# Optimization experiments

Measured on AMD Instinct MI355X. Metric: run time of the kernel, lower is better.

## Reference

```python
import jax, jax.numpy as jnp
import numpy as np

B, S, D, H = 1, 4096, 1024, 16
HD = D // H  # head_size = 64

def setup_inputs() -> dict:
    key = jax.random.key(0)
    ks = jax.random.split(key, 9)
    scale = 1.0 / np.sqrt(D)
    return {
        "x": jax.random.normal(ks[0], (B, S, D), jnp.float32),
        "Wq": jax.random.normal(ks[1], (D, D), jnp.float32) * scale,
        "bq": jax.random.normal(ks[2], (D,), jnp.float32) * 0.01,
        "Wk": jax.random.normal(ks[3], (D, D), jnp.float32) * scale,
        "bk": jax.random.normal(ks[4], (D,), jnp.float32) * 0.01,
        "Wv": jax.random.normal(ks[5], (D, D), jnp.float32) * scale,
        "bv": jax.random.normal(ks[6], (D,), jnp.float32) * 0.01,
        "Wo": jax.random.normal(ks[7], (D, D), jnp.float32) * scale,
        "bo": jax.random.normal(ks[8], (D,), jnp.float32) * 0.01,
    }

def _split_heads(t):
    # (B, S, D) -> (B, H, S, HD)
    return t.reshape(B, S, H, HD).transpose(0, 2, 1, 3)

def reference(x, Wq, bq, Wk, bk, Wv, bv, Wo, bo):
    q = _split_heads(x @ Wq + bq)
    k = _split_heads(x @ Wk + bk)
    v = _split_heads(x @ Wv + bv)
    # scores: (B, H, S, S), materialized as in the original naive attention
    scores = jnp.einsum('bhqd,bhkd->bhqk', q, k) / jnp.sqrt(jnp.asarray(HD, q.dtype))
    causal = jnp.tril(jnp.ones((S, S), dtype=bool))  # tril mask, broadcast over (B, H)
    scores = jnp.where(causal[None, None], scores, jnp.asarray(-1e9, scores.dtype))
    attn = jax.nn.softmax(scores, axis=-1)
    out = jnp.einsum('bhqk,bhkd->bhqd', attn, v)  # (B, H, S, HD)
    out = out.transpose(0, 2, 1, 3).reshape(B, S, D)  # combine heads
    return out @ Wo + bo
```

## Files before the change

### kernel.cpp

```cpp
#include <hip/hip_runtime.h>

#define SEQ 4096
#define DM  1024
#define NH  16
#define HDIM 64

typedef unsigned short u16;
typedef unsigned int   u32;
typedef __bf16 bf16x8 __attribute__((ext_vector_type(8)));
typedef float f32x4 __attribute__((ext_vector_type(4)));

__device__ __forceinline__ float bf2f(u16 u) {
    unsigned v = ((unsigned)u) << 16;
    float f;
    __builtin_memcpy(&f, &v, 4);
    return f;
}
__device__ __forceinline__ u16 f2bf(float f) {
    unsigned u;
    __builtin_memcpy(&u, &f, 4);
    return (u16)((u + 0x7fffu + ((u >> 16) & 1u)) >> 16);
}
__device__ __forceinline__ u32 bfpack(float a, float b) {
    u32 ua, ub;
    __builtin_memcpy(&ua, &a, 4);
    __builtin_memcpy(&ub, &b, 4);
    return ((ua + 0x8000u) >> 16) | ((ub + 0x8000u) & 0xffff0000u);
}

typedef const __attribute__((address_space(1))) unsigned int gas_uint;
typedef __attribute__((address_space(3))) unsigned int las_uint;
__device__ __forceinline__ void gld16(const u16* g, u16* l) {
    __builtin_amdgcn_global_load_lds((gas_uint*)g, (las_uint*)l, 16, 0, 0);
}

__device__ __forceinline__ f32x4 mfma16(bf16x8 a, bf16x8 b, f32x4 c) {
    return __builtin_amdgcn_mfma_f32_16x16x32_bf16(a, b, c, 0, 0, 0);
}

#define QSCALE 0.18033688011f

__global__ __launch_bounds__(256) void detect_k(const u16* __restrict__ w,
                                                int* __restrict__ flags) {
    __shared__ float red[256];
    const int t = threadIdx.x;
    float mx = 0.f;
    for (int i = t; i < 4096; i += 256) {
        float v = fabsf(bf2f(w[i]));
        if (v < 3e38f) mx = fmaxf(mx, v);
    }
    red[t] = mx;
    __syncthreads();
    for (int s = 128; s > 0; s >>= 1) {
        if (t < s) red[t] = fmaxf(red[t], red[t + s]);
        __syncthreads();
    }
    if (t == 0) {
        flags[0] = (red[0] > 1e4f) ? 1 : 0;
        flags[1] = 0;
    }
}

__global__ __launch_bounds__(256) void prep_w(const void* w0, const void* w1,
                                              const void* w2, const void* w3,
                                              const void* b0, const void* b1,
                                              const void* b2, const void* b3,
                                              u16* __restrict__ wt,
                                              u16* __restrict__ b_dst,
                                              const int* __restrict__ flags) {
    __shared__ u16 tile[32][33];
    const int f = flags[0];
    const int z = blockIdx.z;
    const void* win[4] = {w0, w1, w2, w3};
    const void* bin[4] = {b0, b1, b2, b3};
    const void* in = win[z];
    u16* out = wt + (size_t)z * DM * DM;
    const float scale = (z == 0) ? QSCALE : 1.0f;

    const int bx = blockIdx.x * 32;
    const int by = blockIdx.y * 32;
    const int tx = threadIdx.x & 31;
    const int ty = threadIdx.x >> 5;
#pragma unroll
    for (int i = ty; i < 32; i += 8) {
        size_t idx = (size_t)(by + i) * DM + bx + tx;
        float v = f ? ((const float*)in)[idx] : bf2f(((const u16*)in)[idx]);
        tile[i][tx] = f2bf(v * scale);
    }
    __syncthreads();
#pragma unroll
    for (int i = ty; i < 32; i += 8) out[(size_t)(bx + i) * DM + by + tx] = tile[tx][i];

    if (blockIdx.x == 0 && blockIdx.y == 0) {
        const void* bi = bin[z];
        for (int i = threadIdx.x; i < DM; i += 256) {
            float v = f ? ((const float*)bi)[i] : bf2f(((const u16*)bi)[i]);
            b_dst[z * DM + i] = f2bf(v * scale);
        }
    }
}

__global__ __launch_bounds__(256) void cvt_x8(const void* __restrict__ src,
                                              u16* __restrict__ dst,
                                              const int* __restrict__ flags) {
    const size_t i = ((size_t)blockIdx.x * 256 + threadIdx.x) * 8;
    if (flags[0]) {
        const float4* s4 = (const float4*)((const float*)src + i);
        float4 a = s4[0], b = s4[1];
        uint4 o;
        o.x = bfpack(a.x, a.y);
        o.y = bfpack(a.z, a.w);
        o.z = bfpack(b.x, b.y);
        o.w = bfpack(b.z, b.w);
        *(uint4*)(dst + i) = o;
    } else {
        *(uint4*)(dst + i) = *(const uint4*)((const u16*)src + i);
    }
}

__global__ __launch_bounds__(256, 2) void gemm128(const u16* __restrict__ A,
                                                  const u16* __restrict__ Bt,
                                                  const u16* __restrict__ bias,
                                                  void* __restrict__ C0,
                                                  void* __restrict__ C1,
                                                  void* __restrict__ C2,
                                                  int M, int N, int K,
                                                  const int* __restrict__ flags) {
    __shared__ u16 As[128 * 32];
    __shared__ u16 Bs[128 * 32];
    const int f    = flags[0];
    const int tid  = threadIdx.x;
    const int lane = tid & 63;
    const int w    = tid >> 6;
    const int m    = lane & 15;
    const int quad = lane >> 4;
    const int wr   = w >> 1;
    const int wc   = w & 1;
    const int mb = blockIdx.x * 128;
    const int nb = blockIdx.y * 128;
    const int mat = nb >> 10;
    const int lnb = nb & 1023;
    void* C = (mat == 0) ? C0 : ((mat == 1) ? C1 : C2);

    f32x4 acc[4][4] = {};

    for (int kb = 0; kb < K; kb += 32) {
        __syncthreads();
#pragma unroll
        for (int i = 0; i < 2; ++i) {
            const int Lb = i * 256 + w * 64;
            const int L  = Lb + lane;
            const int row = L >> 2, cb = L & 3;
            gld16(&A[(size_t)(mb + row) * K + kb + cb * 8], &As[Lb * 8]);
            gld16(&Bt[(size_t)(nb + row) * K + kb + cb * 8], &Bs[Lb * 8]);
        }
        __syncthreads();

        bf16x8 af[4];
#pragma unroll
        for (int mt = 0; mt < 4; ++mt)
            af[mt] = *(const bf16x8*)&As[(wr * 64 + mt * 16 + m) * 32 + quad * 8];
#pragma unroll
        for (int ct = 0; ct < 4; ++ct) {
            bf16x8 bfr = *(const bf16x8*)&Bs[(wc * 64 + ct * 16 + m) * 32 + quad * 8];
#pragma unroll
            for (int mt = 0; mt < 4; ++mt)
                acc[mt][ct] = mfma16(af[mt], bfr, acc[mt][ct]);
        }
    }

#pragma unroll
    for (int ct = 0; ct < 4; ++ct) {
        float bv = bf2f(bias[nb + wc * 64 + ct * 16 + m]);
#pragma unroll
        for (int mt = 0; mt < 4; ++mt) {
#pragma unroll
            for (int r = 0; r < 4; ++r) {
                int row = mb + wr * 64 + mt * 16 + quad * 4 + r;
                size_t idx = (size_t)row * DM + lnb + wc * 64 + ct * 16 + m;
                float v = acc[mt][ct][r] + bv;
                if (f) ((float*)C)[idx] = v;
                else   ((u16*)C)[idx]   = f2bf(v);
            }
        }
    }
}

__global__ __launch_bounds__(256) void vt_k(const u16* __restrict__ V,
                                            u16* __restrict__ Vt) {
    __shared__ u16 T[64][72];
    const int st = blockIdx.x;
    const int h  = blockIdx.y;
    const int t  = threadIdx.x;
    const int sl = t >> 2, c = t & 3;
    const u16* src = &V[(size_t)(st * 64 + sl) * DM + h * 64 + c * 16];
    *(uint4*)&T[sl][c * 16]     = *(const uint4*)src;
    *(uint4*)&T[sl][c * 16 + 8] = *(const uint4*)(src + 8);
    __syncthreads();
    const int dl = t >> 2, c2 = t & 3;
    u16 tmp[16];
#pragma unroll
    for (int i = 0; i < 16; ++i) tmp[i] = T[c2 * 16 + i][dl];
    u16* dst = &Vt[(size_t)(h * 64 + dl) * SEQ + st * 64 + c2 * 16];
    *(uint4*)dst       = *(const uint4*)&tmp[0];
    *(uint4*)(dst + 8) = *(const uint4*)&tmp[8];
}

__global__ __launch_bounds__(256, 2) void attn_split(const u16* __restrict__ Qb,
                                                     const u16* __restrict__ Kb,
                                                     const u16* __restrict__ Vt,
                                                     u16* __restrict__ slot0,
                                                     u16* __restrict__ slot1,
                                                     u16* __restrict__ slot2,
                                                     float* __restrict__ l0,
                                                     float* __restrict__ l1,
                                                     float* __restrict__ l2) {
    __shared__ u16 Ks[2][64 * 64];
    __shared__ u16 Vs[2][64 * 64];

    const int tid  = threadIdx.x;
    const int lane = tid & 63;
    const int w    = tid >> 6;
    const int m    = lane & 15;
    const int quad = lane >> 4;
    const int l3   = lane >> 3;
    const int cx   = ((lane & 7) ^ l3) * 8;
    const int m7   = m & 7;

    const int b    = blockIdx.x;
    const int x    = b & 7;
    const int u    = b >> 3;
    const int qt2  = 15 - (u / 6);
    const int v6   = u % 6;
    const int head = 2 * x + (v6 / 3);
    const int part = v6 % 3;
    const int hc   = head * HDIM;
    const int n    = 4 * qt2 + 4;
    const int k0t  = part * n / 3;
    const int k1t  = (part + 1) * n / 3 - 1;

    const int qw = qt2 * 256 + w * 64;
    const int dw = qw >> 6;

    bf16x8 qf[4][2];
#pragma unroll
    for (int qt4 = 0; qt4 < 4; ++qt4)
#pragma unroll
        for (int c = 0; c < 2; ++c)
            qf[qt4][c] = *(const bf16x8*)&Qb[(size_t)(qw + qt4 * 16 + m) * DM + hc + c * 32 + quad * 8];

    f32x4 o_acc[4][4] = {};
    float l_part[4] = {0.f, 0.f, 0.f, 0.f};

#pragma unroll
    for (int i = 0; i < 2; ++i) {
        const int r = w * 16 + i * 8 + l3;
        gld16(&Kb[(size_t)(k0t * 64 + r) * DM + hc + cx], &Ks[0][(w * 16 + i * 8) * 64]);
        gld16(&Vt[(size_t)(hc + r) * SEQ + k0t * 64 + cx], &Vs[0][(w * 16 + i * 8) * 64]);
    }

    for (int kt = k0t; kt <= k1t; ++kt) {
        const int cur = (kt - k0t) & 1;
        __syncthreads();

        if (kt < k1t) {
            const int nbf = 1 - cur;
            const int nkt = kt + 1;
#pragma unroll
            for (int i = 0; i < 2; ++i) {
                const int r = w * 16 + i * 8 + l3;
                gld16(&Kb[(size_t)(nkt * 64 + r) * DM + hc + cx], &Ks[nbf][(w * 16 + i * 8) * 64]);
                gld16(&Vt[(size_t)(hc + r) * SEQ + nkt * 64 + cx], &Vs[nbf][(w * 16 + i * 8) * 64]);
            }
        }

        if (kt > dw) continue;

        const u16* ksb = Ks[cur];
        const u16* vsb = Vs[cur];

#pragma unroll
        for (int p = 0; p < 2; ++p) {
            uint4 pa_raw[4];

#pragma unroll
            for (int stt = 0; stt < 2; ++stt) {
                const int st = 2 * p + stt;
                bf16x8 kf[2];
#pragma unroll
                for (int c = 0; c < 2; ++c)
                    kf[c] = *(const bf16x8*)&ksb[(st * 16 + m) * 64 + (((c * 4 + quad) ^ m7) * 8)];

                f32x4 sc[4];
#pragma unroll
                for (int qt4 = 0; qt4 < 4; ++qt4) {
                    f32x4 a = {};
                    a = mfma16(kf[0], qf[qt4][0], a);
                    a = mfma16(kf[1], qf[qt4][1], a);
                    sc[qt4] = a;
                }

                if (kt == dw) {
#pragma unroll
                    for (int qt4 = 0; qt4 < 4; ++qt4)
#pragma unroll
                        for (int r = 0; r < 4; ++r) {
                            float pp = __builtin_amdgcn_exp2f(sc[qt4][r]);
                            sc[qt4][r] = (st * 16 + quad * 4 + r > qt4 * 16 + m) ? 0.f : pp;
                        }
                } else {
#pragma unroll
                    for (int qt4 = 0; qt4 < 4; ++qt4)
#pragma unroll
                        for (int r = 0; r < 4; ++r)
                            sc[qt4][r] = __builtin_amdgcn_exp2f(sc[qt4][r]);
                }

#pragma unroll
                for (int qt4 = 0; qt4 < 4; ++qt4) {
                    l_part[qt4] += sc[qt4][0] + sc[qt4][1] + sc[qt4][2] + sc[qt4][3];
                    const u32 pk0 = bfpack(sc[qt4][0], sc[qt4][1]);
                    const u32 pk1 = bfpack(sc[qt4][2], sc[qt4][3]);
                    if (stt == 0) { pa_raw[qt4].x = pk0; pa_raw[qt4].y = pk1; }
                    else          { pa_raw[qt4].z = pk0; pa_raw[qt4].w = pk1; }
                }
            }

            bf16x8 pa[4];
#pragma unroll
            for (int qt4 = 0; qt4 < 4; ++qt4) __builtin_memcpy(&pa[qt4], &pa_raw[qt4], 16);

#pragma unroll
            for (int dt = 0; dt < 4; ++dt) {
                const int base = (dt * 16 + m) * 64;
                const int clo = ((4 * p + (quad >> 1)) ^ m7) * 8 + (quad & 1) * 4;
                const int chi = ((4 * p + 2 + (quad >> 1)) ^ m7) * 8 + (quad & 1) * 4;
                uint2 vlo = *(const uint2*)&vsb[base + clo];
                uint2 vhi = *(const uint2*)&vsb[base + chi];
                uint4 t;
                t.x = vlo.x; t.y = vlo.y; t.z = vhi.x; t.w = vhi.y;
                bf16x8 vf;
                __builtin_memcpy(&vf, &t, 16);
#pragma unroll
                for (int qt4 = 0; qt4 < 4; ++qt4)
                    o_acc[qt4][dt] = mfma16(pa[qt4], vf, o_acc[qt4][dt]);
            }
        }
    }

#pragma unroll
    for (int qt4 = 0; qt4 < 4; ++qt4) {
        l_part[qt4] += __shfl_xor(l_part[qt4], 16, 64);
        l_part[qt4] += __shfl_xor(l_part[qt4], 32, 64);
    }

    u16*   dst = (part == 0) ? slot0 : ((part == 1) ? slot1 : slot2);
    float* lb  = (part == 0) ? l0 : ((part == 1) ? l1 : l2);
#pragma unroll
    for (int qt4 = 0; qt4 < 4; ++qt4)
#pragma unroll
        for (int dt = 0; dt < 4; ++dt)
#pragma unroll
            for (int r = 0; r < 4; ++r) {
                int row = qw + qt4 * 16 + quad * 4 + r;
                dst[(size_t)row * DM + hc + dt * 16 + m] = f2bf(o_acc[qt4][dt][r]);
            }
    if (lane < 16) {
#pragma unroll
        for (int qt4 = 0; qt4 < 4; ++qt4)
            lb[head * SEQ + qw + qt4 * 16 + lane] = l_part[qt4];
    }
}

__global__ __launch_bounds__(256) void merge_k(u16* __restrict__ s0,
                                               const u16* __restrict__ s1,
                                               const u16* __restrict__ s2,
                                               const float* __restrict__ l0,
                                               const float* __restrict__ l1,
                                               const float* __restrict__ l2) {
    const int gid = blockIdx.x * 256 + threadIdx.x;
    const int rl = gid >> 7;
    const int cg = gid & 127;
    const int h  = cg >> 3;
    const float inv = 1.0f / (l0[h * SEQ + rl] + l1[h * SEQ + rl] + l2[h * SEQ + rl]);
    uint4 va = *(const uint4*)(s0 + (size_t)rl * DM + cg * 8);
    uint4 vb = *(const uint4*)(s1 + (size_t)rl * DM + cg * 8);
    uint4 vc = *(const uint4*)(s2 + (size_t)rl * DM + cg * 8);
    const u16* a16 = (const u16*)&va;
    const u16* b16 = (const u16*)&vb;
    const u16* c16 = (const u16*)&vc;
    u16 oo[8];
#pragma unroll
    for (int i = 0; i < 8; ++i)
        oo[i] = f2bf((bf2f(a16[i]) + bf2f(b16[i]) + bf2f(c16[i])) * inv);
    *(uint4*)(s0 + (size_t)rl * DM + cg * 8) = *(const uint4*)&oo[0];
}

extern "C" void kernel_launch(void* const* d_in, const int* in_sizes, int n_in,
                              void* d_out, int out_size, void* d_ws, size_t ws_size,
                              hipStream_t stream) {
    (void)in_sizes; (void)n_in; (void)out_size; (void)ws_size;

    u16* ws    = (u16*)d_ws;
    int* flags = (int*)d_ws;
    u16* xc    = ws + 64;
    u16* Vt_g  = xc;
    u16* Wtqkv = xc + (size_t)SEQ * DM;
    u16* Wto   = Wtqkv + (size_t)3 * DM * DM;
    u16* bqkv  = Wto + (size_t)DM * DM;
    u16* boc   = bqkv + 3 * DM;
    u16* Qb    = boc + DM;
    u16* Kb    = Qb + (size_t)SEQ * DM;
    u16* Vb    = Kb + (size_t)SEQ * DM;
    u16* ab    = Vb + (size_t)SEQ * DM;
    u16* slotB = ab + (size_t)SEQ * DM;
    u16* slotC = Vb;
    float* l0f = (float*)Wtqkv;
    float* l1f = l0f + NH * SEQ;
    float* l2f = l1f + NH * SEQ;

    detect_k<<<1, 256, 0, stream>>>((const u16*)d_in[1], flags);

    prep_w<<<dim3(DM / 32, DM / 32, 4), 256, 0, stream>>>(
        d_in[1], d_in[3], d_in[5], d_in[7],
        d_in[2], d_in[4], d_in[6], d_in[8],
        Wtqkv, bqkv, flags);

    cvt_x8<<<SEQ * DM / 2048, 256, 0, stream>>>(d_in[0], xc, flags);

    gemm128<<<dim3(SEQ / 128, 3 * DM / 128), 256, 0, stream>>>(
        xc, Wtqkv, bqkv, Qb, Kb, Vb, SEQ, 3 * DM, DM, flags + 1);

    vt_k<<<dim3(SEQ / 64, NH), 256, 0, stream>>>(Vb, Vt_g);

    attn_split<<<dim3(768), 256, 0, stream>>>(Qb, Kb, Vt_g, ab, slotB, slotC,
                                              l0f, l1f, l2f);

    merge_k<<<dim3(SEQ * 128 / 256), 256, 0, stream>>>(ab, slotB, slotC, l0f, l1f, l2f);

    gemm128<<<dim3(SEQ / 128, DM / 128), 256, 0, stream>>>(
        ab, Wto, boc, d_out, d_out, d_out, SEQ, DM, DM, flags);
}
```

Measured before the change: 224.7 us.

## Use 128-key attention tiles and a narrower-N GEMM for output projection

The attention kernel now stages 128 keys per iteration instead of 64, which halves the number of barrier and prefetch steps and doubles the shared-memory tile size. Causal skipping moves to 64-key sub-tiles inside each 128-key tile. The output projection switches to a new 128x64-tile GEMM, giving twice as many blocks so more of the GPU is occupied for the 4096x1024 problem. The costs are roughly double the LDS use in attention, which may reduce occupancy, and coarser work splits per part. The new GEMM has no double buffering.

```diff
diff --git a/kernel.cpp b/kernel.cpp
--- a/kernel.cpp
+++ b/kernel.cpp
@@ -186,6 +186,71 @@
     }
 }
 
+__global__ __launch_bounds__(256, 2) void gemm_n64(const u16* __restrict__ A,
+                                                   const u16* __restrict__ Bt,
+                                                   const u16* __restrict__ bias,
+                                                   void* __restrict__ C,
+                                                   int M, int N, int K,
+                                                   const int* __restrict__ flags) {
+    __shared__ u16 As[128 * 32];
+    __shared__ u16 Bs[64 * 32];
+    const int f    = flags[0];
+    const int tid  = threadIdx.x;
+    const int lane = tid & 63;
+    const int w    = tid >> 6;
+    const int m    = lane & 15;
+    const int quad = lane >> 4;
+    const int mb = blockIdx.x * 128;
+    const int nb = blockIdx.y * 64;
+
+    f32x4 acc[2][4] = {};
+
+    for (int kb = 0; kb < K; kb += 32) {
+        __syncthreads();
+#pragma unroll
+        for (int i = 0; i < 2; ++i) {
+            const int Lb = (2 * w + i) * 64;
+            const int L  = Lb + lane;
+            const int row = L >> 2, cb = L & 3;
+            gld16(&A[(size_t)(mb + row) * K + kb + cb * 8], &As[Lb * 8]);
+        }
+        {
+            const int L = w * 64 + lane;
+            const int row = L >> 2, cb = L & 3;
+            gld16(&Bt[(size_t)(nb + row) * K + kb + cb * 8], &Bs[w * 512]);
+        }
+        __syncthreads();
+
+        bf16x8 af[2];
+#pragma unroll
+        for (int mt = 0; mt < 2; ++mt)
+            af[mt] = *(const bf16x8*)&As[(w * 32 + mt * 16 + m) * 32 + quad * 8];
+#pragma unroll
+        for (int ct = 0; ct < 4; ++ct) {
+            bf16x8 bfr = *(const bf16x8*)&Bs[(ct * 16 + m) * 32 + quad * 8];
+#pragma unroll
+            for (int mt = 0; mt < 2; ++mt)
+                acc[mt][ct] = mfma16(af[mt], bfr, acc[mt][ct]);
+        }
+    }
+
+#pragma unroll
+    for (int ct = 0; ct < 4; ++ct) {
+        float bv = bf2f(bias[nb + ct * 16 + m]);
+#pragma unroll
+        for (int mt = 0; mt < 2; ++mt) {
+#pragma unroll
+            for (int r = 0; r < 4; ++r) {
+                int row = mb + w * 32 + mt * 16 + quad * 4 + r;
+                size_t idx = (size_t)row * N + nb + ct * 16 + m;
+                float v = acc[mt][ct][r] + bv;
+                if (f) ((float*)C)[idx] = v;
+                else   ((u16*)C)[idx]   = f2bf(v);
+            }
+        }
+    }
+}
+
 __global__ __launch_bounds__(256) void vt_k(const u16* __restrict__ V,
                                             u16* __restrict__ Vt) {
     __shared__ u16 T[64][72];
@@ -215,8 +280,8 @@
                                                      float* __restrict__ l0,
                                                      float* __restrict__ l1,
                                                      float* __restrict__ l2) {
-    __shared__ u16 Ks[2][64 * 64];
-    __shared__ u16 Vs[2][64 * 64];
+    __shared__ u16 Ks[2][128 * 64];
+    __shared__ u16 Vs[2][64 * 128];
 
     const int tid  = threadIdx.x;
     const int lane = tid & 63;
@@ -224,8 +289,9 @@
     const int m    = lane & 15;
     const int quad = lane >> 4;
     const int l3   = lane >> 3;
-    const int cx   = ((lane & 7) ^ l3) * 8;
+    const int l4   = lane >> 4;
     const int m7   = m & 7;
+    const int cxk  = ((lane & 7) ^ l3) * 8;
 
     const int b    = blockIdx.x;
     const int x    = b & 7;
@@ -235,9 +301,9 @@
     const int head = 2 * x + (v6 / 3);
     const int part = v6 % 3;
     const int hc   = head * HDIM;
-    const int n    = 4 * qt2 + 4;
-    const int k0t  = part * n / 3;
-    const int k1t  = (part + 1) * n / 3 - 1;
+    const int n128 = 2 * qt2 + 2;
+    const int k0t  = part * n128 / 3;
+    const int k1t  = (part + 1) * n128 / 3 - 1;
 
     const int qw = qt2 * 256 + w * 64;
     const int dw = qw >> 6;
@@ -253,10 +319,12 @@
     float l_part[4] = {0.f, 0.f, 0.f, 0.f};
 
 #pragma unroll
-    for (int i = 0; i < 2; ++i) {
-        const int r = w * 16 + i * 8 + l3;
-        gld16(&Kb[(size_t)(k0t * 64 + r) * DM + hc + cx], &Ks[0][(w * 16 + i * 8) * 64]);
-        gld16(&Vt[(size_t)(hc + r) * SEQ + k0t * 64 + cx], &Vs[0][(w * 16 + i * 8) * 64]);
+    for (int i = 0; i < 4; ++i) {
+        const int kr = w * 32 + i * 8 + l3;
+        gld16(&Kb[(size_t)(k0t * 128 + kr) * DM + hc + cxk], &Ks[0][(w * 32 + i * 8) * 64]);
+        const int vr = w * 16 + i * 4 + l4;
+        const int cxv = ((lane & 15) ^ ((i * 4 + l4) & 7)) * 8;
+        gld16(&Vt[(size_t)(hc + vr) * SEQ + k0t * 128 + cxv], &Vs[0][(w * 16 + i * 4) * 128]);
     }
 
     for (int kt = k0t; kt <= k1t; ++kt) {
@@ -267,83 +335,91 @@
             const int nbf = 1 - cur;
             const int nkt = kt + 1;
 #pragma unroll
-            for (int i = 0; i < 2; ++i) {
-                const int r = w * 16 + i * 8 + l3;
-                gld16(&Kb[(size_t)(nkt * 64 + r) * DM + hc + cx], &Ks[nbf][(w * 16 + i * 8) * 64]);
-                gld16(&Vt[(size_t)(hc + r) * SEQ + nkt * 64 + cx], &Vs[nbf][(w * 16 + i * 8) * 64]);
+            for (int i = 0; i < 4; ++i) {
+                const int kr = w * 32 + i * 8 + l3;
+                gld16(&Kb[(size_t)(nkt * 128 + kr) * DM + hc + cxk], &Ks[nbf][(w * 32 + i * 8) * 64]);
+                const int vr = w * 16 + i * 4 + l4;
+                const int cxv = ((lane & 15) ^ ((i * 4 + l4) & 7)) * 8;
+                gld16(&Vt[(size_t)(hc + vr) * SEQ + nkt * 128 + cxv], &Vs[nbf][(w * 16 + i * 4) * 128]);
             }
         }
-
-        if (kt > dw) continue;
 
         const u16* ksb = Ks[cur];
         const u16* vsb = Vs[cur];
 
 #pragma unroll
-        for (int p = 0; p < 2; ++p) {
-            uint4 pa_raw[4];
-
-#pragma unroll
-            for (int stt = 0; stt < 2; ++stt) {
-                const int st = 2 * p + stt;
-                bf16x8 kf[2];
-#pragma unroll
-                for (int c = 0; c < 2; ++c)
-                    kf[c] = *(const bf16x8*)&ksb[(st * 16 + m) * 64 + (((c * 4 + quad) ^ m7) * 8)];
-
-                f32x4 sc[4];
-#pragma unroll
-                for (int qt4 = 0; qt4 < 4; ++qt4) {
-                    f32x4 a = {};
-                    a = mfma16(kf[0], qf[qt4][0], a);
-                    a = mfma16(kf[1], qf[qt4][1], a);
-                    sc[qt4] = a;
+        for (int h = 0; h < 2; ++h) {
+            const int t64 = kt * 2 + h;
+            if (t64 > dw) continue;
+
+#pragma unroll
+            for (int p = 0; p < 2; ++p) {
+                const int ph = 2 * h + p;
+                uint4 pa_raw[4];
+
+#pragma unroll
+                for (int stt = 0; stt < 2; ++stt) {
+                    const int st = ph * 2 + stt;
+                    bf16x8 kf[2];
+#pragma unroll
+                    for (int c = 0; c < 2; ++c)
+                        kf[c] = *(const bf16x8*)&ksb[(st * 16 + m) * 64 + (((c * 4 + quad) ^ m7) * 8)];
+
+                    f32x4 sc[4];
+#pragma unroll
+                    for (int qt4 = 0; qt4 < 4; ++qt4) {
+                        f32x4 a = {};
+                        a = mfma16(kf[0], qf[qt4][0], a);
+                        a = mfma16(kf[1], qf[qt4][1], a);
+                        sc[qt4] = a;
+                    }
+
+                    if (t64 == dw) {
+                        const int stl = 2 * p + stt;
+#pragma unroll
+                        for (int qt4 = 0; qt4 < 4; ++qt4)
+#pragma unroll
+                            for (int r = 0; r < 4; ++r) {
+                                float pp = __builtin_amdgcn_exp2f(sc[qt4][r]);
+                                sc[qt4][r] = (stl * 16 + quad * 4 + r > qt4 * 16 + m) ? 0.f : pp;
+                            }
+                    } else {
+#pragma unroll
+                        for (int qt4 = 0; qt4 < 4; ++qt4)
+#pragma unroll
+                            for (int r = 0; r < 4; ++r)
+                                sc[qt4][r] = __builtin_amdgcn_exp2f(sc[qt4][r]);
+                    }
+
+#pragma unroll
+                    for (int qt4 = 0; qt4 < 4; ++qt4) {
+                        l_part[qt4] += sc[qt4][0] + sc[qt4][1] + sc[qt4][2] + sc[qt4][3];
+                        const u32 pk0 = bfpack(sc[qt4][0], sc[qt4][1]);
+                        const u32 pk1 = bfpack(sc[qt4][2], sc[qt4][3]);
+                        if (stt == 0) { pa_raw[qt4].x = pk0; pa_raw[qt4].y = pk1; }
+                        else          { pa_raw[qt4].z = pk0; pa_raw[qt4].w = pk1; }
+                    }
                 }
 
-                if (kt == dw) {
+                bf16x8 pa[4];
+#pragma unroll
+                for (int qt4 = 0; qt4 < 4; ++qt4) __builtin_memcpy(&pa[qt4], &pa_raw[qt4], 16);
+
+#pragma unroll
+                for (int dt = 0; dt < 4; ++dt) {
+                    const int base = (dt * 16 + m) * 128;
+                    const int clo = ((4 * ph + (quad >> 1)) ^ m7) * 8 + (quad & 1) * 4;
+                    const int chi = ((4 * ph + 2 + (quad >> 1)) ^ m7) * 8 + (quad & 1) * 4;
+                    uint2 vlo = *(const uint2*)&vsb[base + clo];
+                    uint2 vhi = *(const uint2*)&vsb[base + chi];
+                    uint4 t;
+                    t.x = vlo.x; t.y = vlo.y; t.z = vhi.x; t.w = vhi.y;
+                    bf16x8 vf;
+                    __builtin_memcpy(&vf, &t, 16);
 #pragma unroll
                     for (int qt4 = 0; qt4 < 4; ++qt4)
-#pragma unroll
-                        for (int r = 0; r < 4; ++r) {
-                            float pp = __builtin_amdgcn_exp2f(sc[qt4][r]);
-                            sc[qt4][r] = (st * 16 + quad * 4 + r > qt4 * 16 + m) ? 0.f : pp;
-                        }
-                } else {
-#pragma unroll
-                    for (int qt4 = 0; qt4 < 4; ++qt4)
-#pragma unroll
-                        for (int r = 0; r < 4; ++r)
-                            sc[qt4][r] = __builtin_amdgcn_exp2f(sc[qt4][r]);
+                        o_acc[qt4][dt] = mfma16(pa[qt4], vf, o_acc[qt4][dt]);
                 }
-
-#pragma unroll
-                for (int qt4 = 0; qt4 < 4; ++qt4) {
-                    l_part[qt4] += sc[qt4][0] + sc[qt4][1] + sc[qt4][2] + sc[qt4][3];
-                    const u32 pk0 = bfpack(sc[qt4][0], sc[qt4][1]);
-                    const u32 pk1 = bfpack(sc[qt4][2], sc[qt4][3]);
-                    if (stt == 0) { pa_raw[qt4].x = pk0; pa_raw[qt4].y = pk1; }
-                    else          { pa_raw[qt4].z = pk0; pa_raw[qt4].w = pk1; }
-                }
-            }
-
-            bf16x8 pa[4];
-#pragma unroll
-            for (int qt4 = 0; qt4 < 4; ++qt4) __builtin_memcpy(&pa[qt4], &pa_raw[qt4], 16);
-
-#pragma unroll
-            for (int dt = 0; dt < 4; ++dt) {
-                const int base = (dt * 16 + m) * 64;
-                const int clo = ((4 * p + (quad >> 1)) ^ m7) * 8 + (quad & 1) * 4;
-                const int chi = ((4 * p + 2 + (quad >> 1)) ^ m7) * 8 + (quad & 1) * 4;
-                uint2 vlo = *(const uint2*)&vsb[base + clo];
-                uint2 vhi = *(const uint2*)&vsb[base + chi];
-                uint4 t;
-                t.x = vlo.x; t.y = vlo.y; t.z = vhi.x; t.w = vhi.y;
-                bf16x8 vf;
-                __builtin_memcpy(&vf, &t, 16);
-#pragma unroll
-                for (int qt4 = 0; qt4 < 4; ++qt4)
-                    o_acc[qt4][dt] = mfma16(pa[qt4], vf, o_acc[qt4][dt]);
             }
         }
     }
@@ -438,6 +514,6 @@
 
     merge_k<<<dim3(SEQ * 128 / 256), 256, 0, stream>>>(ab, slotB, slotC, l0f, l1f, l2f);
 
-    gemm128<<<dim3(SEQ / 128, DM / 128), 256, 0, stream>>>(
-        ab, Wto, boc, d_out, d_out, d_out, SEQ, DM, DM, flags);
-}
+    gemm_n64<<<dim3(SEQ / 128, DM / 64), 256, 0, stream>>>(
+        ab, Wto, boc, d_out, SEQ, DM, DM, flags);
+}
```

Measured after the change: 220.5 us. About the same (-1.9%).
